# Optimization experiments

Measured on AMD Instinct MI355X. Metric: run time of the kernel, lower is better.

## Reference

```python
import jax, jax.numpy as jnp
import numpy as np

D_MODEL = 1024
D_INNER = 2048      # expand=2 * d_model
HEADDIM = 64
NHEADS = D_INNER // HEADDIM   # 32 (ssm heads)
D_STATE = 128
D_CONV = 4
CHUNK = 256
D_IN_PROJ = 2 * D_INNER + 2 * D_STATE + NHEADS
CONV_DIM = D_INNER + 2 * D_STATE


def setup_inputs() -> dict:
    key = jax.random.key(0)
    ks = jax.random.split(key, 8)
    sc = lambda f: 1.0 / np.sqrt(f)
    dt_init = jax.random.uniform(ks[3], (NHEADS,), minval=0.001, maxval=0.1)
    return {
        "x": jax.random.normal(ks[0], (2, 4096, D_MODEL), jnp.float32),
        "W_in": jax.random.normal(ks[1], (D_MODEL, D_IN_PROJ), jnp.float32) * sc(D_MODEL),
        "conv_w": jax.random.normal(ks[2], (CONV_DIM, D_CONV), jnp.float32) * sc(D_CONV),
        "conv_b": jnp.zeros((CONV_DIM,), jnp.float32),
        "dt_bias": jnp.log(jnp.expm1(dt_init)),            # inverse softplus
        "A_log": jnp.log(jax.random.uniform(ks[4], (NHEADS,), minval=1.0, maxval=16.0)),
        "D": jnp.ones((NHEADS,), jnp.float32),
        "norm_w": jnp.ones((D_INNER,), jnp.float32),
        "W_out": jax.random.normal(ks[5], (D_INNER, D_MODEL), jnp.float32) * sc(D_INNER),
    }


def _segsum(a):
    # a: (..., T) -> (..., T, T) lower-triangular segment sums, -inf above diag
    T = a.shape[-1]
    cs = jnp.cumsum(a, axis=-1)
    diff = cs[..., :, None] - cs[..., None, :]
    mask = jnp.tril(jnp.ones((T, T), bool))
    return jnp.where(mask, diff, -jnp.inf)


def _ssd(x, A, B, C):
    # x: (b,L,h,p) already scaled by dt; A: (b,L,h) = dt*A_head; B,C: (b,L,n)
    b, L, h, p = x.shape
    nc = L // CHUNK
    xc = x.reshape(b, nc, CHUNK, h, p)
    Ac = A.reshape(b, nc, CHUNK, h).transpose(0, 3, 1, 2)      # (b,h,nc,cl)
    Bc = B.reshape(b, nc, CHUNK, -1)
    Cc = C.reshape(b, nc, CHUNK, -1)
    Acs = jnp.cumsum(Ac, axis=-1)
    # intra-chunk (diagonal) term
    Ldec = jnp.exp(_segsum(Ac))                                # (b,h,nc,cl,cl)
    Yd = jnp.einsum('bcln,bcsn,bhcls,bcshp->bclhp', Cc, Bc, Ldec, xc)
    # chunk end states
    decay_states = jnp.exp(Acs[..., -1:] - Acs)                # (b,h,nc,cl)
    states = jnp.einsum('bcln,bhcl,bclhp->bchpn', Bc, decay_states, xc)
    # inter-chunk recurrence (zero initial state)
    states = jnp.concatenate([jnp.zeros_like(states[:, :1]), states], axis=1)
    A_chunk = jnp.pad(Acs[..., -1], ((0, 0), (0, 0), (1, 0)))  # (b,h,nc+1)
    decay_chunk = jnp.exp(_segsum(A_chunk))                    # (b,h,nc+1,nc+1)
    states = jnp.einsum('bhzc,bchpn->bzhpn', decay_chunk, states)[:, :-1]
    # state -> output term
    out_decay = jnp.exp(Acs)                                   # (b,h,nc,cl)
    Yo = jnp.einsum('bcln,bchpn,bhcl->bclhp', Cc, states, out_decay)
    return (Yd + Yo).reshape(b, L, h, p)


def reference(x, W_in, conv_w, conv_b, dt_bias, A_log, D, norm_w, W_out):
    b, L, _ = x.shape
    zxbcdt = x @ W_in                                          # (b,L,4384)
    z, xBC, dt = jnp.split(zxbcdt, [D_INNER, 2 * D_INNER + 2 * D_STATE], axis=-1)
    # causal depthwise conv1d + silu
    xp = jnp.pad(xBC, ((0, 0), (D_CONV - 1, 0), (0, 0)))
    conv = sum(xp[:, k:k + L] * conv_w[:, k] for k in range(D_CONV)) + conv_b
    xBC = jax.nn.silu(conv)
    xs, B, C = jnp.split(xBC, [D_INNER, D_INNER + D_STATE], axis=-1)
    dt = jax.nn.softplus(dt + dt_bias)                         # (b,L,h)
    A = -jnp.exp(A_log)                                        # (h,)
    xh = xs.reshape(b, L, NHEADS, HEADDIM)
    y = _ssd(xh * dt[..., None], dt * A, B, C)                 # (b,L,h,p)
    y = y + xh * D[None, None, :, None]                        # D skip per head
    y = y.reshape(b, L, D_INNER)
    # gated RMSNorm
    u = y * jax.nn.silu(z)
    u = u * jax.lax.rsqrt(jnp.mean(u * u, axis=-1, keepdims=True) + 1e-5) * norm_w
    return u @ W_out
```

## Files before the change

kernel.cpp:

```cpp
#include <hip/hip_runtime.h>
#include <math.h>

#define B_ 2
#define L_ 4096
#define DM 1024
#define DI 2048
#define HD 64
#define NH 32
#define DS 128
#define CH 256
#define NC 16
#define DPROJ 4384
#define CONVD 2304
#define NGEMM 4352

typedef unsigned short u16;
typedef unsigned int u32;
typedef __attribute__((ext_vector_type(8))) short bf16x8;
typedef __attribute__((ext_vector_type(4))) float f32x4;

__device__ __forceinline__ float silu_(float x) { return x / (1.0f + __expf(-x)); }
__device__ __forceinline__ float us2f(u16 u) {
  union { u32 i; float f; } c; c.i = ((u32)u) << 16; return c.f;
}
__device__ __forceinline__ u16 f2us(float f) {
  union { float f; u32 i; } c; c.f = f;
  u32 i = c.i;
  return (u16)((i + 0x7FFFu + ((i >> 16) & 1u)) >> 16);
}
__device__ __forceinline__ void unpack8(uint4 v, float* o) {
  o[0] = us2f(v.x & 0xffffu); o[1] = us2f(v.x >> 16);
  o[2] = us2f(v.y & 0xffffu); o[3] = us2f(v.y >> 16);
  o[4] = us2f(v.z & 0xffffu); o[5] = us2f(v.z >> 16);
  o[6] = us2f(v.w & 0xffffu); o[7] = us2f(v.w >> 16);
}
__device__ __forceinline__ void unpk16(uint4 v, u16* o) {
  o[0] = (u16)(v.x & 0xffffu); o[1] = (u16)(v.x >> 16);
  o[2] = (u16)(v.y & 0xffffu); o[3] = (u16)(v.y >> 16);
  o[4] = (u16)(v.z & 0xffffu); o[5] = (u16)(v.z >> 16);
  o[6] = (u16)(v.w & 0xffffu); o[7] = (u16)(v.w >> 16);
}
__device__ __forceinline__ bf16x8 scale8(bf16x8 a, float s) {
  bf16x8 r;
#pragma unroll
  for (int j = 0; j < 8; ++j) r[j] = (short)f2us(us2f((u16)a[j]) * s);
  return r;
}
__device__ __forceinline__ void gload16(const u16* g, u16* l) {
  __builtin_amdgcn_global_load_lds(
      (const __attribute__((address_space(1))) void*)g,
      (__attribute__((address_space(3))) void*)l, 16, 0, 0);
}

__global__ __launch_bounds__(256) void prep_k(const float* __restrict__ x,
                                              const float* __restrict__ W_in,
                                              const float* __restrict__ W_out,
                                              const float* __restrict__ nw,
                                              const float* __restrict__ dtb,
                                              float* __restrict__ dtp,
                                              u16* __restrict__ xb16,
                                              u16* __restrict__ wint,
                                              u16* __restrict__ woutt) {
  __shared__ float shmem[8 * 1024];
  const int t = threadIdx.x;
  const int bid = blockIdx.x;
  if (bid < 1024) {
    const int row0 = bid * 8;
#pragma unroll
    for (int i = 0; i < 8; ++i) {
      int j4 = i * 256 + t;
      float4 v = *(const float4*)&x[(size_t)row0 * DM + j4 * 4];
      *(float4*)&shmem[j4 * 4] = v;
      u32 lo = (u32)f2us(v.x) | ((u32)f2us(v.y) << 16);
      u32 hi = (u32)f2us(v.z) | ((u32)f2us(v.w) << 16);
      *(uint2*)&xb16[(size_t)row0 * DM + j4 * 4] = make_uint2(lo, hi);
    }
    __syncthreads();
    const int r = t >> 5, h = t & 31;
    float a0 = 0.f, a1 = 0.f, a2 = 0.f, a3 = 0.f;
    const float* wcol = W_in + (DI + CONVD) + h;
    const float* xr = &shmem[r * 1024];
    for (int k = 0; k < 1024; k += 4) {
      float4 xv = *(const float4*)&xr[k];
      a0 += xv.x * wcol[(size_t)(k + 0) * DPROJ];
      a1 += xv.y * wcol[(size_t)(k + 1) * DPROJ];
      a2 += xv.z * wcol[(size_t)(k + 2) * DPROJ];
      a3 += xv.w * wcol[(size_t)(k + 3) * DPROJ];
    }
    float v = (a0 + a1) + (a2 + a3) + dtb[h];
    dtp[(size_t)(row0 + r) * NH + h] = (v > 20.0f) ? v : log1pf(__expf(v));
  } else {
    float (*tile)[65] = (float(*)[65])shmem;
    const float* W; u16* Wt; int ldW, ldT, n0, k0; bool fold;
    if (bid < 2112) {
      int j = bid - 1024;
      W = W_in; Wt = wint; ldW = DPROJ; ldT = DM; fold = false;
      n0 = (j % (NGEMM / 64)) * 64; k0 = (j / (NGEMM / 64)) * 64;
    } else {
      int j = bid - 2112;
      W = W_out; Wt = woutt; ldW = DM; ldT = DI; fold = true;
      n0 = (j % (DM / 64)) * 64; k0 = (j / (DM / 64)) * 64;
    }
#pragma unroll
    for (int i = 0; i < 16; ++i) {
      int j = i * 256 + t;
      int kk = j >> 6, nn = j & 63;
      float v = W[(size_t)(k0 + kk) * ldW + n0 + nn];
      if (fold) v *= nw[k0 + kk];
      tile[kk][nn] = v;
    }
    __syncthreads();
#pragma unroll
    for (int i = 0; i < 16; ++i) {
      int j = i * 256 + t;
      int nn = j >> 6, kk = j & 63;
      Wt[(size_t)(n0 + nn) * ldT + k0 + kk] = f2us(tile[kk][nn]);
    }
  }
}

__global__ __launch_bounds__(512, 4) void gemm_in_k(const u16* __restrict__ A,
                                                    const u16* __restrict__ Bt,
                                                    u16* __restrict__ zb,
                                                    u16* __restrict__ xraw,
                                                    int nwg) {
  __shared__ u16 pool[24576];
  u16* Al = pool;
  u16* Bl = pool + 16384;
  const int t = threadIdx.x;
  const int w = t >> 6, lane = t & 63;
  const int fr = lane & 15, oct = lane >> 4;
  const int wm = w >> 1, wn = w & 1;
  const int q = nwg >> 3;
  const int wg = (blockIdx.x & 7) * q + (blockIdx.x >> 3);
  const int bm = wg / (NGEMM / 128), bn = wg % (NGEMM / 128);
  const int m0 = bm * 256, n0 = bn * 128;
  const int lr = lane >> 3, ls = lane & 7;
  const int gslot = (ls ^ lr) * 8;

  f32x4 acc[4][4];
#pragma unroll
  for (int mm = 0; mm < 4; ++mm)
#pragma unroll
    for (int nn = 0; nn < 4; ++nn) acc[mm][nn] = (f32x4){0.f, 0.f, 0.f, 0.f};

  for (int k0 = 0; k0 < DM; k0 += 64) {
    if (k0) __syncthreads();
#pragma unroll
    for (int i = 0; i < 4; ++i) {
      const int rowA = w * 32 + i * 8;
      gload16(&A[(size_t)(m0 + rowA + lr) * DM + k0 + gslot], &Al[rowA * 64]);
    }
#pragma unroll
    for (int i = 0; i < 2; ++i) {
      const int rowB = w * 16 + i * 8;
      gload16(&Bt[(size_t)(n0 + rowB + lr) * DM + k0 + gslot], &Bl[rowB * 64]);
    }
    __syncthreads();
#pragma unroll
    for (int kk = 0; kk < 2; ++kk) {
      bf16x8 af[4], bfr[4];
#pragma unroll
      for (int mm = 0; mm < 4; ++mm)
        af[mm] = *(const bf16x8*)&Al[(wm * 64 + mm * 16 + fr) * 64 +
                                     (((kk * 4 + oct) ^ (fr & 7)) * 8)];
#pragma unroll
      for (int nn = 0; nn < 4; ++nn)
        bfr[nn] = *(const bf16x8*)&Bl[(wn * 64 + nn * 16 + fr) * 64 +
                                      (((kk * 4 + oct) ^ (fr & 7)) * 8)];
      __builtin_amdgcn_s_setprio(1);
#pragma unroll
      for (int mm = 0; mm < 4; ++mm)
#pragma unroll
        for (int nn = 0; nn < 4; ++nn)
          acc[mm][nn] = __builtin_amdgcn_mfma_f32_16x16x32_bf16(af[mm], bfr[nn],
                                                                acc[mm][nn], 0, 0, 0);
      __builtin_amdgcn_s_setprio(0);
    }
  }

  const bool isz = (n0 < DI);
  u16* Oh = pool;
#pragma unroll
  for (int P = 0; P < 4; ++P) {
    __syncthreads();
    if (wm == P) {
#pragma unroll
      for (int mm = 0; mm < 4; ++mm)
#pragma unroll
        for (int i = 0; i < 4; ++i) {
          int rloc = mm * 16 + oct * 4 + i;
#pragma unroll
          for (int nn = 0; nn < 4; ++nn)
            Oh[rloc * 136 + wn * 64 + nn * 16 + fr] = f2us(acc[mm][nn][i]);
        }
    }
    __syncthreads();
#pragma unroll
    for (int p = 0; p < 2; ++p) {
      int e = p * 512 + t;
      int row = e >> 4, cs = (e & 15) * 8;
      uint4 v = *(const uint4*)&Oh[row * 136 + cs];
      size_t grow = m0 + P * 64 + row;
      int col = n0 + cs;
      if (isz) *(uint4*)&zb[grow * DI + col] = v;
      else     *(uint4*)&xraw[grow * CONVD + (col - DI)] = v;
    }
  }
}

template <int KDIM, int NTN>
__global__ __launch_bounds__(256) void gemm_out_k(const u16* __restrict__ A,
                                                  const u16* __restrict__ Bt,
                                                  const float* __restrict__ psum,
                                                  float* __restrict__ outf,
                                                  int nwg) {
  __shared__ u16 pool[17408];
  __shared__ float rs_s[128];
  u16* Al = pool;
  u16* Bl = pool + 8192;
  const int t = threadIdx.x;
  const int wv = t >> 6, lane = t & 63;
  const int fr = lane & 15, oct = lane >> 4;
  const int wr = wv >> 1, wc = wv & 1;
  const int q = nwg >> 3;
  const int wg = (blockIdx.x & 7) * q + (blockIdx.x >> 3);
  const int bm = wg / NTN, bn = wg % NTN;
  const int m0 = bm * 128, n0 = bn * 128;

  if (t < 128) {
    const float4* p = (const float4*)&psum[(size_t)(m0 + t) * 32];
    float s = 0.0f;
#pragma unroll
    for (int i = 0; i < 8; ++i) {
      float4 v = p[i];
      s += (v.x + v.y) + (v.z + v.w);
    }
    rs_s[t] = rsqrtf(s * (1.0f / DI) + 1e-5f);
  }

  const int lr = lane >> 3, ls = lane & 7;
  const int gslot = (ls ^ lr) * 8;

  f32x4 acc[4][4];
#pragma unroll
  for (int mm = 0; mm < 4; ++mm)
#pragma unroll
    for (int nn = 0; nn < 4; ++nn) acc[mm][nn] = (f32x4){0.f, 0.f, 0.f, 0.f};

  for (int k0 = 0; k0 < KDIM; k0 += 64) {
    if (k0) __syncthreads();
#pragma unroll
    for (int i = 0; i < 4; ++i) {
      const int rowA = wv * 32 + i * 8;
      gload16(&A[(size_t)(m0 + rowA + lr) * KDIM + k0 + gslot], &Al[rowA * 64]);
      gload16(&Bt[(size_t)(n0 + rowA + lr) * KDIM + k0 + gslot], &Bl[rowA * 64]);
    }
    __syncthreads();
#pragma unroll
    for (int kk = 0; kk < 2; ++kk) {
      bf16x8 af[4], bfr[4];
#pragma unroll
      for (int mm = 0; mm < 4; ++mm)
        af[mm] = *(const bf16x8*)&Al[(wr * 64 + mm * 16 + fr) * 64 +
                                     (((kk * 4 + oct) ^ (fr & 7)) * 8)];
#pragma unroll
      for (int nn = 0; nn < 4; ++nn)
        bfr[nn] = *(const bf16x8*)&Bl[(wc * 64 + nn * 16 + fr) * 64 +
                                      (((kk * 4 + oct) ^ (fr & 7)) * 8)];
#pragma unroll
      for (int mm = 0; mm < 4; ++mm)
#pragma unroll
        for (int nn = 0; nn < 4; ++nn)
          acc[mm][nn] = __builtin_amdgcn_mfma_f32_16x16x32_bf16(af[mm], bfr[nn],
                                                                acc[mm][nn], 0, 0, 0);
    }
  }

#pragma unroll
  for (int P = 0; P < 2; ++P) {
    __syncthreads();
    float* Of = (float*)pool;
    if (wr == P) {
#pragma unroll
      for (int mm = 0; mm < 4; ++mm)
#pragma unroll
        for (int i = 0; i < 4; ++i) {
          int rloc = mm * 16 + oct * 4 + i;
#pragma unroll
          for (int nn = 0; nn < 4; ++nn)
            Of[rloc * 132 + wc * 64 + nn * 16 + fr] = acc[mm][nn][i];
        }
    }
    __syncthreads();
#pragma unroll
    for (int p = 0; p < 8; ++p) {
      int e = p * 256 + t;
      int row = e >> 5, c4 = (e & 31) * 4;
      float s = rs_s[P * 64 + row];
      float4 v = *(const float4*)&Of[row * 132 + c4];
      v.x *= s; v.y *= s; v.z *= s; v.w *= s;
      *(float4*)&outf[(size_t)(m0 + P * 64 + row) * DM + n0 + c4] = v;
    }
  }
}

__global__ __launch_bounds__(256) void conv_silu_k(const u16* __restrict__ xraw,
                                                   const float* __restrict__ cw,
                                                   const float* __restrict__ cb,
                                                   u16* __restrict__ xbc) {
  int idx = blockIdx.x * 256 + threadIdx.x;
  int ch8 = idx % (CONVD / 8);
  int bl = idx / (CONVD / 8);
  int l = bl & (L_ - 1);
  int ch = ch8 * 8;
  const u16* src = xraw + (size_t)bl * CONVD + ch;
  float a[8], o[8];
#pragma unroll
  for (int qq = 0; qq < 8; ++qq) a[qq] = cb[ch + qq];
  float w0[8], w1[8], w2[8], w3[8];
#pragma unroll
  for (int qq = 0; qq < 8; ++qq) {
    float4 w = *(const float4*)&cw[(ch + qq) * 4];
    w0[qq] = w.x; w1[qq] = w.y; w2[qq] = w.z; w3[qq] = w.w;
  }
  if (l >= 3) {
    uint4 v = *(const uint4*)&src[-3 * CONVD]; unpack8(v, o);
#pragma unroll
    for (int qq = 0; qq < 8; ++qq) a[qq] += o[qq] * w0[qq];
  }
  if (l >= 2) {
    uint4 v = *(const uint4*)&src[-2 * CONVD]; unpack8(v, o);
#pragma unroll
    for (int qq = 0; qq < 8; ++qq) a[qq] += o[qq] * w1[qq];
  }
  if (l >= 1) {
    uint4 v = *(const uint4*)&src[-CONVD]; unpack8(v, o);
#pragma unroll
    for (int qq = 0; qq < 8; ++qq) a[qq] += o[qq] * w2[qq];
  }
  {
    uint4 v = *(const uint4*)&src[0]; unpack8(v, o);
#pragma unroll
    for (int qq = 0; qq < 8; ++qq) a[qq] += o[qq] * w3[qq];
  }
  uint4 ov;
  ov.x = (u32)f2us(silu_(a[0])) | ((u32)f2us(silu_(a[1])) << 16);
  ov.y = (u32)f2us(silu_(a[2])) | ((u32)f2us(silu_(a[3])) << 16);
  ov.z = (u32)f2us(silu_(a[4])) | ((u32)f2us(silu_(a[5])) << 16);
  ov.w = (u32)f2us(silu_(a[6])) | ((u32)f2us(silu_(a[7])) << 16);
  *(uint4*)&xbc[(size_t)bl * CONVD + ch] = ov;
}

#define SLP 72
__global__ __launch_bounds__(256) void states_k(const u16* __restrict__ xbc,
                                                const float* __restrict__ dtp,
                                                const float* __restrict__ A_log,
                                                float* __restrict__ Acs,
                                                u16* __restrict__ st16) {
  __shared__ u16 BtT[128 * SLP];
  __shared__ u16 XtT[64 * SLP];
  __shared__ float acs_s[256];
  const int t = threadIdx.x;
  const int wv = t >> 6, lane = t & 63;
  const int fr = lane & 15, oct = lane >> 4;
  const int sw = (blockIdx.x & 7) * 128 + (blockIdx.x >> 3);
  const int h = sw & 31, c = (sw >> 5) & 15, b = sw >> 9;
  const size_t acsb = (((size_t)b * NH + h) * NC + c) * CH;
  const size_t rowbase = (size_t)b * L_ + c * CH;

  if (t < 64) {
    const float Ah = -__expf(A_log[h]);
    const size_t base = (rowbase + t * 4) * NH + h;
    float v0 = dtp[base] * Ah;
    float v1 = dtp[base + NH] * Ah;
    float v2 = dtp[base + 2 * NH] * Ah;
    float v3 = dtp[base + 3 * NH] * Ah;
    float c1 = v0 + v1, c2 = c1 + v2, c3 = c2 + v3;
    float tot = c3;
#pragma unroll
    for (int off = 1; off < 64; off <<= 1) {
      float p = __shfl_up(tot, off, 64);
      if (t >= off) tot += p;
    }
    float excl = tot - c3;
    float4 ov = make_float4(excl + v0, excl + c1, excl + c2, excl + c3);
    *(float4*)&acs_s[t * 4] = ov;
    *(float4*)&Acs[acsb + t * 4] = ov;
  }
  __syncthreads();
  const float acs_last = acs_s[255];

  f32x4 acc[2][4];
#pragma unroll
  for (int mt = 0; mt < 2; ++mt)
#pragma unroll
    for (int pt = 0; pt < 4; ++pt) acc[mt][pt] = (f32x4){0.f, 0.f, 0.f, 0.f};

  for (int lt = 0; lt < 4; ++lt) {
    __syncthreads();
#pragma unroll
    for (int i = 0; i < 2; ++i) {
      int ci = i * 256 + t;
      int lp = ci >> 4, nk = ci & 15;
      int l0 = lp * 2;
      const u16* srcp = &xbc[(rowbase + lt * 64 + l0) * CONVD + DI + nk * 8];
      uint4 v0 = *(const uint4*)srcp;
      uint4 v1 = *(const uint4*)(srcp + CONVD);
      u16 a0[8], a1[8];
      unpk16(v0, a0); unpk16(v1, a1);
#pragma unroll
      for (int qq = 0; qq < 8; ++qq) {
        int r = nk * 8 + qq;
        u32 val = (u32)a0[qq] | ((u32)a1[qq] << 16);
        *(u32*)&BtT[r * SLP + ((((l0 >> 3) ^ (r >> 3)) & 7) << 3) + (l0 & 7)] = val;
      }
    }
    {
      int lp = t >> 3, pk = t & 7;
      int l0 = lp * 2;
      size_t row0 = rowbase + lt * 64 + l0;
      uint4 v0 = *(const uint4*)&xbc[row0 * CONVD + h * HD + pk * 8];
      uint4 v1 = *(const uint4*)&xbc[(row0 + 1) * CONVD + h * HD + pk * 8];
      float d0 = dtp[row0 * NH + h] * __expf(acs_last - acs_s[lt * 64 + l0]);
      float d1 = dtp[(row0 + 1) * NH + h] * __expf(acs_last - acs_s[lt * 64 + l0 + 1]);
      float o0[8], o1[8];
      unpack8(v0, o0); unpack8(v1, o1);
#pragma unroll
      for (int qq = 0; qq < 8; ++qq) {
        int r = pk * 8 + qq;
        u32 val = (u32)f2us(o0[qq] * d0) | ((u32)f2us(o1[qq] * d1) << 16);
        *(u32*)&XtT[r * SLP + ((((l0 >> 3) ^ (r >> 3)) & 7) << 3) + (l0 & 7)] = val;
      }
    }
    __syncthreads();
    __builtin_amdgcn_s_setprio(1);
#pragma unroll
    for (int ks = 0; ks < 2; ++ks) {
      bf16x8 afr[2], bfr[4];
#pragma unroll
      for (int mt = 0; mt < 2; ++mt) {
        int r = wv * 32 + mt * 16 + fr;
        afr[mt] = *(const bf16x8*)&BtT[r * SLP + ((((ks * 4 + oct) ^ (r >> 3)) & 7) << 3)];
      }
#pragma unroll
      for (int pt = 0; pt < 4; ++pt) {
        int r = pt * 16 + fr;
        bfr[pt] = *(const bf16x8*)&XtT[r * SLP + ((((ks * 4 + oct) ^ (r >> 3)) & 7) << 3)];
      }
#pragma unroll
      for (int mt = 0; mt < 2; ++mt)
#pragma unroll
        for (int pt = 0; pt < 4; ++pt)
          acc[mt][pt] = __builtin_amdgcn_mfma_f32_16x16x32_bf16(afr[mt], bfr[pt],
                                                                acc[mt][pt], 0, 0, 0);
    }
    __builtin_amdgcn_s_setprio(0);
  }
  size_t sbase = (((size_t)b * NC + c) * NH + h) * (size_t)(HD * DS);
#pragma unroll
  for (int mt = 0; mt < 2; ++mt)
#pragma unroll
    for (int pt = 0; pt < 4; ++pt) {
      int p = pt * 16 + fr;
      int n0 = wv * 32 + mt * 16 + oct * 4;
      u32 lo = (u32)f2us(acc[mt][pt][0]) | ((u32)f2us(acc[mt][pt][1]) << 16);
      u32 hi = (u32)f2us(acc[mt][pt][2]) | ((u32)f2us(acc[mt][pt][3]) << 16);
      *(uint2*)&st16[sbase + (size_t)p * DS + n0] = make_uint2(lo, hi);
    }
}

__global__ __launch_bounds__(256) void scan_k(u16* __restrict__ st16,
                                              const float* __restrict__ Acs) {
  const int t = threadIdx.x;
  const int seg = blockIdx.x & 15;
  const int bh = blockIdx.x >> 4;
  const int h = bh & 31, b = bh >> 5;
  const int e2 = seg * 256 + t;
  const size_t acssb = ((size_t)b * NH + h) * NC * CH;
  float run0 = 0.0f, run1 = 0.0f;
#pragma unroll
  for (int c = 0; c < NC; ++c) {
    float dAl = __expf(Acs[acssb + (size_t)c * CH + (CH - 1)]);
    size_t e = (((size_t)b * NC + c) * NH + h) * (size_t)(HD * DS) + e2 * 2;
    u32 v = *(const u32*)&st16[e];
    float s0 = us2f((u16)(v & 0xffffu)), s1 = us2f((u16)(v >> 16));
    *(u32*)&st16[e] = (u32)f2us(run0) | ((u32)f2us(run1) << 16);
    run0 = fmaf(dAl, run0, s0);
    run1 = fmaf(dAl, run1, s1);
  }
}

#define SP 72
#define XOFF 8192
#define POFF 12800
__global__ __launch_bounds__(512, 4) void ssd_out_k(const u16* __restrict__ xbc,
                                                    const float* __restrict__ dtp,
                                                    const float* __restrict__ Acs,
                                                    const u16* __restrict__ st16,
                                                    const float* __restrict__ Dvec,
                                                    const u16* __restrict__ zb,
                                                    u16* __restrict__ v_out,
                                                    float* __restrict__ psum) {
  __shared__ u16 pool[31232];
  __shared__ float acs_s[256];
  const int t = threadIdx.x;
  const int w = t >> 6, lane = t & 63;
  const int fr = lane & 15, oct = lane >> 4;
  const int sw = (blockIdx.x & 7) * 128 + (blockIdx.x >> 3);
  const int h = sw & 31, c = (sw >> 5) & 15, b = sw >> 9;
  const size_t acsb = (((size_t)b * NH + h) * NC + c) * CH;
  const size_t rowbase = (size_t)b * L_ + c * CH;
  if (t < 256) acs_s[t] = Acs[acsb + t];
  const size_t sb = (((size_t)b * NC + c) * NH + h) * (size_t)(HD * DS);
#pragma unroll
  for (int i = 0; i < 2; ++i) {
    int ci = i * 512 + t; int p = ci >> 4, nk = ci & 15;
    uint4 v = *(const uint4*)&st16[sb + (size_t)p * DS + nk * 8];
    *(uint4*)&pool[p * 136 + nk * 8] = v;
  }
  __syncthreads();
  bf16x8 ca[2][4];
#pragma unroll
  for (int mt = 0; mt < 2; ++mt)
#pragma unroll
    for (int kk = 0; kk < 4; ++kk)
      ca[mt][kk] = *(const bf16x8*)&xbc[(rowbase + w * 32 + mt * 16 + fr) * CONVD +
                                        DI + DS + kk * 32 + oct * 8];
  f32x4 acc_y[2][4];
#pragma unroll
  for (int mt = 0; mt < 2; ++mt)
#pragma unroll
    for (int pp4 = 0; pp4 < 4; ++pp4) acc_y[mt][pp4] = (f32x4){0.f, 0.f, 0.f, 0.f};

  {
    float eL0 = __expf(acs_s[w * 32 + fr]);
    float eL1 = __expf(acs_s[w * 32 + 16 + fr]);
    __builtin_amdgcn_s_setprio(1);
#pragma unroll
    for (int kk = 0; kk < 4; ++kk) {
      bf16x8 c0 = scale8(ca[0][kk], eL0);
      bf16x8 c1 = scale8(ca[1][kk], eL1);
#pragma unroll
      for (int pp4 = 0; pp4 < 4; ++pp4) {
        bf16x8 sf = *(const bf16x8*)&pool[(pp4 * 16 + fr) * 136 + kk * 32 + oct * 8];
        acc_y[0][pp4] = __builtin_amdgcn_mfma_f32_16x16x32_bf16(c0, sf, acc_y[0][pp4], 0, 0, 0);
        acc_y[1][pp4] = __builtin_amdgcn_mfma_f32_16x16x32_bf16(c1, sf, acc_y[1][pp4], 0, 0, 0);
      }
    }
    __builtin_amdgcn_s_setprio(0);
  }

  const int stmax = w >> 1, delta = (w & 1) << 5;
  for (int st = 0; st < 4; ++st) {
    __syncthreads();
#pragma unroll
    for (int i = 0; i < 2; ++i) {
      int ci = i * 512 + t; int ll = ci >> 4, ck = ci & 15;
      uint4 v = *(const uint4*)&xbc[(rowbase + st * 64 + ll) * CONVD + DI + ck * 8];
      *(uint4*)&pool[ll * 128 + ((ck * 8) ^ ((ll & 7) << 3))] = v;
    }
    if (t < 256) {
      int lp = t >> 3, pk = t & 7;
      int s0 = lp * 2;
      size_t row0 = rowbase + st * 64 + s0;
      uint4 v0 = *(const uint4*)&xbc[row0 * CONVD + h * HD + pk * 8];
      uint4 v1 = *(const uint4*)&xbc[(row0 + 1) * CONVD + h * HD + pk * 8];
      float d0 = dtp[row0 * NH + h];
      float d1 = dtp[(row0 + 1) * NH + h];
      float o0[8], o1[8];
      unpack8(v0, o0); unpack8(v1, o1);
#pragma unroll
      for (int qq = 0; qq < 8; ++qq) {
        int r = pk * 8 + qq;
        u32 val = (u32)f2us(o0[qq] * d0) | ((u32)f2us(o1[qq] * d1) << 16);
        *(u32*)&pool[XOFF + r * SP + ((((s0 >> 3) ^ (r >> 3)) & 7) << 3) + (s0 & 7)] = val;
      }
    }
    __syncthreads();
    if (st > stmax) continue;
    const bool diag = (st == stmax);
#pragma unroll
    for (int ss4 = 0; ss4 < 4; ++ss4) {
      bf16x8 bbf[4];
#pragma unroll
      for (int kk = 0; kk < 4; ++kk)
        bbf[kk] = *(const bf16x8*)&pool[(ss4 * 16 + fr) * 128 +
                                        ((kk * 32 + oct * 8) ^ ((fr & 7) << 3))];
      int s_in = ss4 * 16 + fr;
      float aS = acs_s[st * 64 + s_in];
#pragma unroll
      for (int mt = 0; mt < 2; ++mt) {
        f32x4 sacc = (f32x4){0.f, 0.f, 0.f, 0.f};
        __builtin_amdgcn_s_setprio(1);
#pragma unroll
        for (int kk = 0; kk < 4; ++kk)
          sacc = __builtin_amdgcn_mfma_f32_16x16x32_bf16(ca[mt][kk], bbf[kk], sacc, 0, 0, 0);
        __builtin_amdgcn_s_setprio(0);
#pragma unroll
        for (int i = 0; i < 4; ++i) {
          int r = mt * 16 + oct * 4 + i;
          float aL = acs_s[w * 32 + r];
          float wgt = (!diag || (s_in <= r + delta)) ? __expf(aL - aS) : 0.0f;
          pool[POFF + w * 2304 + r * SP + s_in] = f2us(sacc[i] * wgt);
        }
      }
    }
    bf16x8 pa[2][2];
#pragma unroll
    for (int mt = 0; mt < 2; ++mt)
#pragma unroll
      for (int k2 = 0; k2 < 2; ++k2)
        pa[mt][k2] = *(const bf16x8*)&pool[POFF + w * 2304 + (mt * 16 + fr) * SP +
                                           k2 * 32 + oct * 8];
    __builtin_amdgcn_s_setprio(1);
#pragma unroll
    for (int pp4 = 0; pp4 < 4; ++pp4) {
      int rx = pp4 * 16 + fr, xg = rx >> 3;
      bf16x8 xb0 = *(const bf16x8*)&pool[XOFF + rx * SP + (((oct) ^ xg) & 7) * 8];
      bf16x8 xb1 = *(const bf16x8*)&pool[XOFF + rx * SP + (((4 + oct) ^ xg) & 7) * 8];
#pragma unroll
      for (int mt = 0; mt < 2; ++mt) {
        acc_y[mt][pp4] = __builtin_amdgcn_mfma_f32_16x16x32_bf16(pa[mt][0], xb0, acc_y[mt][pp4], 0, 0, 0);
        acc_y[mt][pp4] = __builtin_amdgcn_mfma_f32_16x16x32_bf16(pa[mt][1], xb1, acc_y[mt][pp4], 0, 0, 0);
      }
    }
    __builtin_amdgcn_s_setprio(0);
  }

  const float Dh = Dvec[h];
  float rs[2][4];
#pragma unroll
  for (int mt = 0; mt < 2; ++mt)
#pragma unroll
    for (int i = 0; i < 4; ++i) {
      size_t row = rowbase + w * 32 + mt * 16 + oct * 4 + i;
      float rsum = 0.0f;
#pragma unroll
      for (int pp4 = 0; pp4 < 4; ++pp4) {
        int col = h * HD + pp4 * 16 + fr;
        float xs = us2f(xbc[row * CONVD + col]);
        float zz = us2f(zb[row * DI + col]);
        float vv = (acc_y[mt][pp4][i] + Dh * xs) * silu_(zz);
        v_out[row * DI + col] = f2us(vv);
        rsum += vv * vv;
      }
      rs[mt][i] = rsum;
    }
#pragma unroll
  for (int mt = 0; mt < 2; ++mt)
#pragma unroll
    for (int i = 0; i < 4; ++i) {
      float s = rs[mt][i];
#pragma unroll
      for (int off = 8; off >= 1; off >>= 1) s += __shfl_xor(s, off, 64);
      if (fr == 0) {
        size_t row = rowbase + w * 32 + mt * 16 + oct * 4 + i;
        psum[row * 32 + h] = s;
      }
    }
}

extern "C" void kernel_launch(void* const* d_in, const int* in_sizes, int n_in,
                              void* d_out, int out_size, void* d_ws, size_t ws_size,
                              hipStream_t stream) {
  const float* x      = (const float*)d_in[0];
  const float* W_in   = (const float*)d_in[1];
  const float* conv_w = (const float*)d_in[2];
  const float* conv_b = (const float*)d_in[3];
  const float* dt_b   = (const float*)d_in[4];
  const float* A_log  = (const float*)d_in[5];
  const float* Dvec   = (const float*)d_in[6];
  const float* norm_w = (const float*)d_in[7];
  const float* W_out  = (const float*)d_in[8];
  float* out = (float*)d_out;

  u16* zb       = (u16*)d_ws;
  u16* xbc      = zb + (size_t)B_ * L_ * DI;
  float* dtp    = (float*)(xbc + (size_t)B_ * L_ * CONVD);
  float* Acs    = dtp + (size_t)B_ * L_ * NH;
  u16* stregion = (u16*)(Acs + (size_t)B_ * NH * L_);
  u16* uni      = stregion + (size_t)B_ * NC * NH * HD * DS * 2;
  u16* xraw = uni;
  u16* v    = uni;

  u16* xb16     = stregion;
  u16* wint     = stregion + (size_t)B_ * L_ * DM;
  u16* woutt    = wint + (size_t)NGEMM * DM;
  float* psum   = (float*)(woutt + (size_t)DM * DI);
  u16* states16 = stregion;

  const int Mrows = B_ * L_;

  prep_k<<<1024 + (NGEMM / 64) * (DM / 64) + (DM / 64) * (DI / 64), 256, 0, stream>>>(
      x, W_in, W_out, norm_w, dt_b, dtp, xb16, wint, woutt);

  const int nwg_in = (Mrows / 256) * (NGEMM / 128);
  gemm_in_k<<<nwg_in, 512, 0, stream>>>(xb16, wint, zb, xraw, nwg_in);

  conv_silu_k<<<(Mrows * (CONVD / 8)) / 256, 256, 0, stream>>>(xraw, conv_w, conv_b, xbc);
  states_k<<<B_ * NC * NH, 256, 0, stream>>>(xbc, dtp, A_log, Acs, states16);
  scan_k<<<B_ * NH * 16, 256, 0, stream>>>(states16, Acs);
  ssd_out_k<<<B_ * NC * NH, 512, 0, stream>>>(xbc, dtp, Acs, states16, Dvec,
                                              zb, v, psum);

  const int nwg_out = (Mrows / 128) * (DM / 128);
  gemm_out_k<DI, DM / 128><<<nwg_out, 256, 0, stream>>>(v, woutt, psum, out, nwg_out);
}
```

Before: 337.4 us.

## Fuse causal conv1d and SiLU into input GEMM epilogue with boundary fixup kernel

The causal depthwise conv and SiLU move into the in-projection GEMM epilogue. The staged bf16 output tile in shared memory is reused, and the last three rows of each 64-row sub-tile are carried into the next one. Only the first three rows of each 256-row tile are written raw to global memory, and a small fixup kernel computes those boundary rows afterwards. This removes a full read and write pass over the conv activations and one full-size launch. In exchange the GEMM epilogue gets extra shared memory traffic, conv arithmetic and boundary logic.

```diff
diff --git a/kernel.cpp b/kernel.cpp
--- a/kernel.cpp
+++ b/kernel.cpp
@@ -121,8 +121,11 @@
 
 __global__ __launch_bounds__(512, 4) void gemm_in_k(const u16* __restrict__ A,
                                                     const u16* __restrict__ Bt,
+                                                    const float* __restrict__ cw,
+                                                    const float* __restrict__ cb,
                                                     u16* __restrict__ zb,
                                                     u16* __restrict__ xraw,
+                                                    u16* __restrict__ xbc,
                                                     int nwg) {
   __shared__ u16 pool[24576];
   u16* Al = pool;
@@ -180,7 +183,9 @@
   }
 
   const bool isz = (n0 < DI);
+  const int chb = n0 - DI;
   u16* Oh = pool;
+  u16* prev3 = pool + 8704;
 #pragma unroll
   for (int P = 0; P < 4; ++P) {
     __syncthreads();
@@ -202,11 +207,75 @@
       int row = e >> 4, cs = (e & 15) * 8;
       uint4 v = *(const uint4*)&Oh[row * 136 + cs];
       size_t grow = m0 + P * 64 + row;
-      int col = n0 + cs;
-      if (isz) *(uint4*)&zb[grow * DI + col] = v;
-      else     *(uint4*)&xraw[grow * CONVD + (col - DI)] = v;
-    }
-  }
+      if (isz) {
+        *(uint4*)&zb[grow * DI + n0 + cs] = v;
+      } else {
+        const int ccol = chb + cs;
+        if ((P == 0 && row < 3) || (P == 3 && row >= 61))
+          *(uint4*)&xraw[grow * CONVD + ccol] = v;
+        if (P > 0 || row >= 3) {
+          u16 rr[4][8];
+#pragma unroll
+          for (int k = 0; k < 4; ++k) {
+            int rsrc = row - 3 + k;
+            const u16* srow = (rsrc >= 0) ? &Oh[rsrc * 136] : &prev3[(3 + rsrc) * 136];
+            *(uint4*)rr[k] = *(const uint4*)&srow[cs];
+          }
+          float a[8];
+#pragma unroll
+          for (int qq = 0; qq < 8; ++qq) {
+            float4 wv = *(const float4*)&cw[(ccol + qq) * 4];
+            a[qq] = cb[ccol + qq] + us2f(rr[0][qq]) * wv.x + us2f(rr[1][qq]) * wv.y +
+                    us2f(rr[2][qq]) * wv.z + us2f(rr[3][qq]) * wv.w;
+          }
+          uint4 ov;
+          ov.x = (u32)f2us(silu_(a[0])) | ((u32)f2us(silu_(a[1])) << 16);
+          ov.y = (u32)f2us(silu_(a[2])) | ((u32)f2us(silu_(a[3])) << 16);
+          ov.z = (u32)f2us(silu_(a[4])) | ((u32)f2us(silu_(a[5])) << 16);
+          ov.w = (u32)f2us(silu_(a[6])) | ((u32)f2us(silu_(a[7])) << 16);
+          *(uint4*)&xbc[grow * CONVD + ccol] = ov;
+        }
+      }
+    }
+    __syncthreads();
+    if (!isz && t < 51) {
+      int r = t / 17, c8 = (t % 17) * 8;
+      *(uint4*)&prev3[r * 136 + c8] = *(const uint4*)&Oh[(61 + r) * 136 + c8];
+    }
+  }
+}
+
+__global__ __launch_bounds__(256) void conv_fix_k(const u16* __restrict__ xraw,
+                                                  const float* __restrict__ cw,
+                                                  const float* __restrict__ cb,
+                                                  u16* __restrict__ xbc) {
+  int idx = blockIdx.x * 256 + threadIdx.x;
+  if (idx >= 96 * (CONVD / 8)) return;
+  int colg = idx % (CONVD / 8);
+  int rid = idx / (CONVD / 8);
+  size_t l = (size_t)(rid / 3) * 256 + (rid % 3);
+  int lb = (int)(l & (L_ - 1));
+  int ch = colg * 8;
+  const u16* src = xraw + l * CONVD + ch;
+  float a[8], o[8];
+#pragma unroll
+  for (int qq = 0; qq < 8; ++qq) a[qq] = cb[ch + qq];
+#pragma unroll
+  for (int k = 0; k < 4; ++k) {
+    int dl = 3 - k;
+    if (lb >= dl) {
+      uint4 v = *(const uint4*)(src - (size_t)dl * CONVD);
+      unpack8(v, o);
+#pragma unroll
+      for (int qq = 0; qq < 8; ++qq) a[qq] += o[qq] * cw[(ch + qq) * 4 + k];
+    }
+  }
+  uint4 ov;
+  ov.x = (u32)f2us(silu_(a[0])) | ((u32)f2us(silu_(a[1])) << 16);
+  ov.y = (u32)f2us(silu_(a[2])) | ((u32)f2us(silu_(a[3])) << 16);
+  ov.z = (u32)f2us(silu_(a[4])) | ((u32)f2us(silu_(a[5])) << 16);
+  ov.w = (u32)f2us(silu_(a[6])) | ((u32)f2us(silu_(a[7])) << 16);
+  *(uint4*)&xbc[l * CONVD + ch] = ov;
 }
 
 template <int KDIM, int NTN>
@@ -303,53 +372,6 @@
       *(float4*)&outf[(size_t)(m0 + P * 64 + row) * DM + n0 + c4] = v;
     }
   }
-}
-
-__global__ __launch_bounds__(256) void conv_silu_k(const u16* __restrict__ xraw,
-                                                   const float* __restrict__ cw,
-                                                   const float* __restrict__ cb,
-                                                   u16* __restrict__ xbc) {
-  int idx = blockIdx.x * 256 + threadIdx.x;
-  int ch8 = idx % (CONVD / 8);
-  int bl = idx / (CONVD / 8);
-  int l = bl & (L_ - 1);
-  int ch = ch8 * 8;
-  const u16* src = xraw + (size_t)bl * CONVD + ch;
-  float a[8], o[8];
-#pragma unroll
-  for (int qq = 0; qq < 8; ++qq) a[qq] = cb[ch + qq];
-  float w0[8], w1[8], w2[8], w3[8];
-#pragma unroll
-  for (int qq = 0; qq < 8; ++qq) {
-    float4 w = *(const float4*)&cw[(ch + qq) * 4];
-    w0[qq] = w.x; w1[qq] = w.y; w2[qq] = w.z; w3[qq] = w.w;
-  }
-  if (l >= 3) {
-    uint4 v = *(const uint4*)&src[-3 * CONVD]; unpack8(v, o);
-#pragma unroll
-    for (int qq = 0; qq < 8; ++qq) a[qq] += o[qq] * w0[qq];
-  }
-  if (l >= 2) {
-    uint4 v = *(const uint4*)&src[-2 * CONVD]; unpack8(v, o);
-#pragma unroll
-    for (int qq = 0; qq < 8; ++qq) a[qq] += o[qq] * w1[qq];
-  }
-  if (l >= 1) {
-    uint4 v = *(const uint4*)&src[-CONVD]; unpack8(v, o);
-#pragma unroll
-    for (int qq = 0; qq < 8; ++qq) a[qq] += o[qq] * w2[qq];
-  }
-  {
-    uint4 v = *(const uint4*)&src[0]; unpack8(v, o);
-#pragma unroll
-    for (int qq = 0; qq < 8; ++qq) a[qq] += o[qq] * w3[qq];
-  }
-  uint4 ov;
-  ov.x = (u32)f2us(silu_(a[0])) | ((u32)f2us(silu_(a[1])) << 16);
-  ov.y = (u32)f2us(silu_(a[2])) | ((u32)f2us(silu_(a[3])) << 16);
-  ov.z = (u32)f2us(silu_(a[4])) | ((u32)f2us(silu_(a[5])) << 16);
-  ov.w = (u32)f2us(silu_(a[6])) | ((u32)f2us(silu_(a[7])) << 16);
-  *(uint4*)&xbc[(size_t)bl * CONVD + ch] = ov;
 }
 
 #define SLP 72
@@ -696,9 +718,10 @@
       x, W_in, W_out, norm_w, dt_b, dtp, xb16, wint, woutt);
 
   const int nwg_in = (Mrows / 256) * (NGEMM / 128);
-  gemm_in_k<<<nwg_in, 512, 0, stream>>>(xb16, wint, zb, xraw, nwg_in);
-
-  conv_silu_k<<<(Mrows * (CONVD / 8)) / 256, 256, 0, stream>>>(xraw, conv_w, conv_b, xbc);
+  gemm_in_k<<<nwg_in, 512, 0, stream>>>(xb16, wint, conv_w, conv_b, zb, xraw, xbc, nwg_in);
+
+  conv_fix_k<<<(96 * (CONVD / 8) + 255) / 256, 256, 0, stream>>>(xraw, conv_w, conv_b, xbc);
+
   states_k<<<B_ * NC * NH, 256, 0, stream>>>(xbc, dtp, A_log, Acs, states16);
   scan_k<<<B_ * NH * 16, 256, 0, stream>>>(states16, Acs);
   ssd_out_k<<<B_ * NC * NH, 512, 0, stream>>>(xbc, dtp, Acs, states16, Dvec,
```

New measurement: 418.9 us, median of 2. 24.2% more time.
